# Performance work log

Hardware: AMD Instinct MI355X
Metric: run time of the kernel (lower is better)

The kernel has to match this reference:

```python
import jax, jax.numpy as jnp
import numpy as np

H_DIM = 2048
N_HEADS = 16

def setup_inputs() -> dict:
    key = jax.random.key(0)
    ks = jax.random.split(key, 9)
    B, T, C = 2, 2048, H_DIM
    scale = 1.0 / np.sqrt(C)  # lecun_normal approx
    src = jax.random.normal(ks[0], (B, T, C), dtype=jnp.float32)
    Wq = jax.random.normal(ks[1], (C, H_DIM), dtype=jnp.float32) * scale
    Wk = jax.random.normal(ks[2], (C, H_DIM), dtype=jnp.float32) * scale
    Wv = jax.random.normal(ks[3], (C, H_DIM), dtype=jnp.float32) * scale
    Wo = jax.random.normal(ks[4], (H_DIM, H_DIM), dtype=jnp.float32) * scale
    bq = jnp.zeros((H_DIM,), jnp.float32)
    bk = jnp.zeros((H_DIM,), jnp.float32)
    bv = jnp.zeros((H_DIM,), jnp.float32)
    bo = jnp.zeros((H_DIM,), jnp.float32)
    return {"src": src, "Wq": Wq, "bq": bq, "Wk": Wk, "bk": bk,
            "Wv": Wv, "bv": bv, "Wo": Wo, "bo": bo}

def reference(src, Wq, bq, Wk, bk, Wv, bv, Wo, bo):
    B, T, C = src.shape
    N = N_HEADS
    D = C // N
    def heads(x):  # [B,T,h_dim] -> [B,N,T,D]
        return x.reshape(B, T, N, D).transpose(0, 2, 1, 3)
    q = heads(src @ Wq + bq)
    k = heads(src @ Wk + bk)
    v = heads(src @ Wv + bv)
    # scaled dot-product with causal mask
    scores = jnp.einsum('bntd,bnsd->bnts', q, k) / jnp.sqrt(jnp.float32(D))
    causal = jnp.tril(jnp.ones((T, T), dtype=bool))
    scores = jnp.where(causal[None, None], scores, -jnp.inf)
    attn = jax.nn.softmax(scores, axis=-1)
    out = jnp.einsum('bnts,bnsd->bntd', attn, v)  # dropout is identity (drop_p=0)
    out = out.transpose(0, 2, 1, 3).reshape(B, T, N * D)
    return out @ Wo + bo
```

## Files before the change

kernel.cpp:

```cpp
#include <hip/hip_runtime.h>
#include <hip/hip_bf16.h>

typedef float f32x4 __attribute__((ext_vector_type(4)));
typedef __bf16 bf16x8v __attribute__((ext_vector_type(8)));
typedef __bf16 bf16x4v __attribute__((ext_vector_type(4)));
typedef unsigned uint2v __attribute__((ext_vector_type(2)));
typedef bf16x8v __attribute__((may_alias)) bf16x8;
typedef bf16x4v __attribute__((may_alias)) bf16x4;
typedef uint2v __attribute__((may_alias)) u32x2;

typedef __attribute__((address_space(1))) const void gvoid_t;
typedef __attribute__((address_space(3))) void lvoid_t;

#define DEVINL __device__ __forceinline__

#define BDIM 2
#define TDIM 2048
#define CDIM 2048
#define NHEAD 16
#define DHEAD 128
#define MROWS 4096
#define WSZ ((size_t)CDIM * CDIM)
#define XSZ ((size_t)MROWS * CDIM)

#define BARRIER_LGKM() asm volatile("s_waitcnt lgkmcnt(0)\ns_barrier" ::: "memory")

DEVINL __bf16 f2bf(float f) {
  unsigned u = __builtin_bit_cast(unsigned, f);
  u += 0x7fffu + ((u >> 16) & 1u);
  unsigned short h = (unsigned short)(u >> 16);
  return __builtin_bit_cast(__bf16, h);
}

DEVINL unsigned pk2bf_trunc(float lo, float hi) {
  return __builtin_amdgcn_perm(__builtin_bit_cast(unsigned, hi),
                               __builtin_bit_cast(unsigned, lo), 0x07060302);
}

DEVINL void gl2lds16(const void* g, void* l) {
  __builtin_amdgcn_global_load_lds((gvoid_t*)g, (lvoid_t*)l, 16, 0, 0);
}

__global__ void detect_dtype(const unsigned* __restrict__ w,
                             int* __restrict__ flag, int* __restrict__ cnt) {
  const int l = threadIdx.x;
  if (l == 0) *cnt = 0;
  const unsigned word = w[l];
  const unsigned e = (word >> 7) & 0xFFu;
  const int vote = (e >= 0x70u && e <= 0x87u) ? 1 : 0;
  const unsigned long long m = __ballot(vote);
  if (l == 0) *flag = (__popcll(m) >= 32) ? 1 : 0;
}

__global__ __launch_bounds__(256) void cvt_src(const void* __restrict__ in,
                                               __bf16* __restrict__ out,
                                               const int* __restrict__ flag,
                                               int n8) {
  const int i = blockIdx.x * 256 + threadIdx.x;
  if (i >= n8) return;
  if (*flag) {
    ((bf16x8*)out)[i] = ((const bf16x8*)in)[i];
  } else {
    const float* f = (const float*)in + (size_t)i * 8;
    bf16x8v v;
#pragma unroll
    for (int j = 0; j < 8; ++j) v[j] = f2bf(f[j]);
    ((bf16x8*)out)[i] = v;
  }
}

__global__ __launch_bounds__(256) void cvt_wt(
    const void* __restrict__ w0, const void* __restrict__ w1,
    const void* __restrict__ w2, const void* __restrict__ w3,
    __bf16* __restrict__ out, const int* __restrict__ flag) {
  __shared__ __attribute__((aligned(16))) __bf16 tile[64][68];
  const void* W = (blockIdx.z == 0) ? w0 : (blockIdx.z == 1) ? w1
                : (blockIdx.z == 2) ? w2 : w3;
  __bf16* Wt = out + (size_t)blockIdx.z * WSZ;
  const int tx = threadIdx.x & 63, ty = threadIdx.x >> 6;
  const int k0 = blockIdx.x * 64, n0 = blockIdx.y * 64;
  const int fl = *flag;
#pragma unroll
  for (int i = ty; i < 64; i += 4) {
    const size_t off = (size_t)(k0 + i) * CDIM + n0 + tx;
    const float v = fl ? (float)((const __bf16*)W)[off] : ((const float*)W)[off];
    tile[i][tx] = f2bf(v);
  }
  __syncthreads();
#pragma unroll
  for (int i = ty; i < 64; i += 4)
    Wt[(size_t)(n0 + i) * CDIM + k0 + tx] = tile[tx][i];
}

__global__ __launch_bounds__(256) void cvt_bias(
    const void* __restrict__ b0, const void* __restrict__ b1,
    const void* __restrict__ b2, const void* __restrict__ b3,
    float* __restrict__ out, const int* __restrict__ flag) {
  const int i = blockIdx.x * 256 + threadIdx.x;
  const void* b = (i < 2048) ? b0 : (i < 4096) ? b1 : (i < 6144) ? b2 : b3;
  const int idx = i & 2047;
  out[i] = (*flag) ? (float)((const __bf16*)b)[idx] : ((const float*)b)[idx];
}

__global__ __launch_bounds__(256) void gemm_qkv(
    const __bf16* __restrict__ A, const __bf16* __restrict__ Bt,
    const float* __restrict__ bias, __bf16* __restrict__ qb,
    __bf16* __restrict__ kb, __bf16* __restrict__ vtb) {
  constexpr int K = CDIM;
  __shared__ __attribute__((aligned(16))) __bf16 Als[128 * 32];
  __shared__ __attribute__((aligned(16))) __bf16 Bls[128 * 32];
  const int tid = threadIdx.x;
  const int w = tid >> 6, l = tid & 63;
  const int quad = l >> 4, l16 = l & 15;
  const int wm = (w >> 1) * 64, wn = (w & 1) * 64;
  const int m0 = blockIdx.x * 128, n0 = blockIdx.y * 128;

  f32x4 acc[4][4];
#pragma unroll
  for (int i = 0; i < 4; ++i)
#pragma unroll
    for (int j = 0; j < 4; ++j) acc[i][j] = (f32x4){0.f, 0.f, 0.f, 0.f};

  const int srow = w * 32 + (l >> 2);
  const int swz = (l & 3) ^ ((l >> 3) & 3);
  const __bf16* ga = A + (size_t)(m0 + srow) * K + swz * 8;
  const __bf16* gb = Bt + (size_t)(n0 + srow) * K + swz * 8;
  __bf16* la = Als + w * 1024;
  __bf16* lb = Bls + w * 1024;
  const int cswz = (quad ^ ((l16 >> 1) & 3)) * 8;

  for (int k0 = 0; k0 < K; k0 += 32) {
    __syncthreads();
#pragma unroll
    for (int j = 0; j < 2; ++j) {
      gl2lds16(ga + (size_t)j * 16 * K + k0, la + j * 512);
      gl2lds16(gb + (size_t)j * 16 * K + k0, lb + j * 512);
    }
    __syncthreads();
    bf16x8 af[4], bfr[4];
#pragma unroll
    for (int i = 0; i < 4; ++i)
      af[i] = *(const bf16x8*)&Als[(wm + i * 16 + l16) * 32 + cswz];
#pragma unroll
    for (int j = 0; j < 4; ++j)
      bfr[j] = *(const bf16x8*)&Bls[(wn + j * 16 + l16) * 32 + cswz];
#pragma unroll
    for (int i = 0; i < 4; ++i)
#pragma unroll
      for (int j = 0; j < 4; ++j)
        acc[i][j] = __builtin_amdgcn_mfma_f32_16x16x32_bf16(af[i], bfr[j],
                                                            acc[i][j], 0, 0, 0);
  }

  const int mat = n0 >> 11;
#pragma unroll
  for (int j = 0; j < 4; ++j) {
    const int n = n0 + wn + j * 16 + l16;
    const int nn = n & 2047;
    const int h = nn >> 7, d = nn & 127;
    const float bv = bias[n];
#pragma unroll
    for (int i = 0; i < 4; ++i) {
      const int mbase = m0 + wm + i * 16 + quad * 4;
      const int bb = mbase >> 11, t = mbase & 2047;
      if (mat == 2) {
        bf16x4v v4;
#pragma unroll
        for (int r = 0; r < 4; ++r) v4[r] = f2bf(acc[i][j][r] + bv);
        *(bf16x4*)&vtb[((size_t)(bb * NHEAD + h) * DHEAD + d) * TDIM + t] = v4;
      } else {
        __bf16* outp = (mat == 0) ? qb : kb;
#pragma unroll
        for (int r = 0; r < 4; ++r)
          outp[((size_t)(bb * NHEAD + h) * TDIM + t + r) * DHEAD + d] =
              f2bf(acc[i][j][r] + bv);
      }
    }
  }
}

__global__ __launch_bounds__(256) void gemm_out(
    const __bf16* __restrict__ A, const __bf16* __restrict__ Bt,
    const float* __restrict__ bias, void* __restrict__ outp,
    const int* __restrict__ flag) {
  constexpr int K = CDIM;
  __shared__ __attribute__((aligned(16))) __bf16 Als[128 * 32];
  __shared__ __attribute__((aligned(16))) __bf16 Bls[128 * 32];
  const int tid = threadIdx.x;
  const int w = tid >> 6, l = tid & 63;
  const int quad = l >> 4, l16 = l & 15;
  const int wm = (w >> 1) * 64, wn = (w & 1) * 64;
  const int m0 = blockIdx.x * 128, n0 = blockIdx.y * 128;
  const int ofl = *flag;

  f32x4 acc[4][4];
#pragma unroll
  for (int i = 0; i < 4; ++i)
#pragma unroll
    for (int j = 0; j < 4; ++j) acc[i][j] = (f32x4){0.f, 0.f, 0.f, 0.f};

  const int srow = w * 32 + (l >> 2);
  const int swz = (l & 3) ^ ((l >> 3) & 3);
  const __bf16* ga = A + (size_t)(m0 + srow) * K + swz * 8;
  const __bf16* gb = Bt + (size_t)(n0 + srow) * K + swz * 8;
  __bf16* la = Als + w * 1024;
  __bf16* lb = Bls + w * 1024;
  const int cswz = (quad ^ ((l16 >> 1) & 3)) * 8;

  for (int k0 = 0; k0 < K; k0 += 32) {
    __syncthreads();
#pragma unroll
    for (int j = 0; j < 2; ++j) {
      gl2lds16(ga + (size_t)j * 16 * K + k0, la + j * 512);
      gl2lds16(gb + (size_t)j * 16 * K + k0, lb + j * 512);
    }
    __syncthreads();
    bf16x8 af[4], bfr[4];
#pragma unroll
    for (int i = 0; i < 4; ++i)
      af[i] = *(const bf16x8*)&Als[(wm + i * 16 + l16) * 32 + cswz];
#pragma unroll
    for (int j = 0; j < 4; ++j)
      bfr[j] = *(const bf16x8*)&Bls[(wn + j * 16 + l16) * 32 + cswz];
#pragma unroll
    for (int i = 0; i < 4; ++i)
#pragma unroll
      for (int j = 0; j < 4; ++j)
        acc[i][j] = __builtin_amdgcn_mfma_f32_16x16x32_bf16(af[i], bfr[j],
                                                            acc[i][j], 0, 0, 0);
  }

#pragma unroll
  for (int j = 0; j < 4; ++j) {
    const int n = n0 + wn + j * 16 + l16;
    const float bv = bias[n];
#pragma unroll
    for (int i = 0; i < 4; ++i) {
#pragma unroll
      for (int r = 0; r < 4; ++r) {
        const int m = m0 + wm + i * 16 + quad * 4 + r;
        const float v = acc[i][j][r] + bv;
        if (ofl) ((__bf16*)outp)[(size_t)m * CDIM + n] = f2bf(v);
        else     ((float*)outp)[(size_t)m * CDIM + n] = v;
      }
    }
  }
}

__global__ __launch_bounds__(256, 2) void attn(
    const __bf16* __restrict__ Q, const __bf16* __restrict__ K,
    const __bf16* __restrict__ Vt, __bf16* __restrict__ ctx,
    int* __restrict__ cnt) {
  constexpr float CSC = 0.12753139726f;
  __shared__ __attribute__((aligned(16))) __bf16 Kls[64 * 128];
  __shared__ __attribute__((aligned(16))) __bf16 Vls[128 * 64];
  __shared__ __attribute__((aligned(16))) __bf16 Pls[4][32 * 64];
  __shared__ int jobLds;

  const int tid = threadIdx.x;
  const int w = tid >> 6, l = tid & 63, quad = l >> 4, l16 = l & 15;

  const int krow = tid >> 4;
  const int kcol = tid & 15;
  const int kldsoff = ((kcol ^ krow) * 8);
  const int vrow = tid >> 3;
  const int vcol = tid & 7;
  const int vldsoff = ((vcol ^ (vrow & 7)) * 8);

  for (;;) {
    __syncthreads();
    if (tid == 0) jobLds = atomicAdd(cnt, 1);
    __syncthreads();
    const int j = jobLds;
    if (j >= 512) break;
    const int qt = 15 - (j >> 5);
    const int bh = j & 31;
    const int t0w = qt * 128 + w * 32;
    const __bf16* Qbh = Q + (size_t)bh * TDIM * DHEAD;
    const __bf16* Kbh = K + (size_t)bh * TDIM * DHEAD;
    const __bf16* Vbh = Vt + (size_t)bh * TDIM * DHEAD;

    bf16x8 qf[2][4];
#pragma unroll
    for (int tt = 0; tt < 2; ++tt)
#pragma unroll
      for (int ks = 0; ks < 4; ++ks)
        qf[tt][ks] = *(const bf16x8*)(Qbh +
                     (size_t)(t0w + tt * 16 + l16) * DHEAD + ks * 32 + quad * 8);

    f32x4 oacc[8][2];
#pragma unroll
    for (int dt = 0; dt < 8; ++dt)
#pragma unroll
      for (int tt = 0; tt < 2; ++tt) oacc[dt][tt] = (f32x4){0.f, 0.f, 0.f, 0.f};
    float mrow[2] = {-1e30f, -1e30f};
    float lrow[2] = {0.f, 0.f};

    const int nsb = 2 * (qt + 1);

    bf16x8 kr[4], vr[4];
#pragma unroll
    for (int p = 0; p < 4; ++p)
      kr[p] = *(const bf16x8*)(Kbh + (size_t)(p * 16 + krow) * DHEAD + kcol * 8);
#pragma unroll
    for (int p = 0; p < 4; ++p)
      vr[p] = *(const bf16x8*)(Vbh + (size_t)(p * 32 + vrow) * TDIM + vcol * 8);

    for (int sb = 0; sb < nsb; ++sb) {
      const int s0 = sb * 64;
      BARRIER_LGKM();
#pragma unroll
      for (int p = 0; p < 4; ++p)
        *(bf16x8*)&Kls[(p * 16 + krow) * 128 + kldsoff] = kr[p];
#pragma unroll
      for (int p = 0; p < 4; ++p)
        *(bf16x8*)&Vls[(p * 32 + vrow) * 64 + vldsoff] = vr[p];
      if (sb + 1 < nsb) {
        const int s1 = s0 + 64;
#pragma unroll
        for (int p = 0; p < 4; ++p)
          kr[p] = *(const bf16x8*)(Kbh + (size_t)(s1 + p * 16 + krow) * DHEAD +
                                   kcol * 8);
#pragma unroll
        for (int p = 0; p < 4; ++p)
          vr[p] = *(const bf16x8*)(Vbh + (size_t)(p * 32 + vrow) * TDIM + s1 +
                                   vcol * 8);
      }
      BARRIER_LGKM();
      if (s0 > t0w + 31) continue;

      f32x4 sacc[4][2];
#pragma unroll
      for (int st = 0; st < 4; ++st)
#pragma unroll
        for (int tt = 0; tt < 2; ++tt) sacc[st][tt] = (f32x4){0.f, 0.f, 0.f, 0.f};
#pragma unroll
      for (int ks = 0; ks < 4; ++ks) {
        bf16x8 kf[4];
#pragma unroll
        for (int st = 0; st < 4; ++st)
          kf[st] = *(const bf16x8*)&Kls[(st * 16 + l16) * 128 +
                                        (((ks * 4 + quad) ^ l16) * 8)];
#pragma unroll
        for (int st = 0; st < 4; ++st)
#pragma unroll
          for (int tt = 0; tt < 2; ++tt)
            sacc[st][tt] = __builtin_amdgcn_mfma_f32_16x16x32_bf16(
                kf[st], qf[tt][ks], sacc[st][tt], 0, 0, 0);
      }
      if (s0 + 63 > t0w) {
#pragma unroll
        for (int st = 0; st < 4; ++st)
#pragma unroll
          for (int tt = 0; tt < 2; ++tt)
#pragma unroll
            for (int r = 0; r < 4; ++r) {
              const int s = s0 + st * 16 + quad * 4 + r;
              const int t = t0w + tt * 16 + l16;
              if (s > t) sacc[st][tt][r] = -1e30f;
            }
      }
#pragma unroll
      for (int tt = 0; tt < 2; ++tt) {
        float vm = -1e30f;
#pragma unroll
        for (int st = 0; st < 4; ++st)
#pragma unroll
          for (int r = 0; r < 4; ++r) vm = fmaxf(vm, sacc[st][tt][r]);
        vm = fmaxf(vm, __shfl_xor(vm, 16));
        vm = fmaxf(vm, __shfl_xor(vm, 32));
        const float mnew = fmaxf(mrow[tt], vm);
        if (__ballot(mnew > mrow[tt])) {
          const float alpha = exp2f((mrow[tt] - mnew) * CSC);
          lrow[tt] *= alpha;
#pragma unroll
          for (int dt = 0; dt < 8; ++dt)
#pragma unroll
            for (int r = 0; r < 4; ++r) oacc[dt][tt][r] *= alpha;
          mrow[tt] = mnew;
        }
        float rs = 0.f;
#pragma unroll
        for (int st = 0; st < 4; ++st) {
          const float p0 = exp2f((sacc[st][tt][0] - mnew) * CSC);
          const float p1 = exp2f((sacc[st][tt][1] - mnew) * CSC);
          const float p2 = exp2f((sacc[st][tt][2] - mnew) * CSC);
          const float p3 = exp2f((sacc[st][tt][3] - mnew) * CSC);
          rs += (p0 + p1) + (p2 + p3);
          u32x2 pk = {pk2bf_trunc(p0, p1), pk2bf_trunc(p2, p3)};
          *(u32x2*)&Pls[w][(tt * 16 + l16) * 64 +
                           (((st * 2 + (quad >> 1)) ^ (l16 & 7)) * 8) +
                           (quad & 1) * 4] = pk;
        }
        rs += __shfl_xor(rs, 16);
        rs += __shfl_xor(rs, 32);
        lrow[tt] += rs;
      }
      asm volatile("s_waitcnt lgkmcnt(0)" ::: "memory");
#pragma unroll
      for (int ks = 0; ks < 2; ++ks) {
        bf16x8 pf[2];
#pragma unroll
        for (int tt = 0; tt < 2; ++tt)
          pf[tt] = *(const bf16x8*)&Pls[w][(tt * 16 + l16) * 64 +
                                           (((ks * 4 + quad) ^ (l16 & 7)) * 8)];
#pragma unroll
        for (int dt = 0; dt < 8; ++dt) {
          const bf16x8 vf =
              *(const bf16x8*)&Vls[(dt * 16 + l16) * 64 +
                                   (((ks * 4 + quad) ^ (l16 & 7)) * 8)];
#pragma unroll
          for (int tt = 0; tt < 2; ++tt)
            oacc[dt][tt] = __builtin_amdgcn_mfma_f32_16x16x32_bf16(
                vf, pf[tt], oacc[dt][tt], 0, 0, 0);
        }
      }
    }

    const int b = bh >> 4, h = bh & 15;
#pragma unroll
    for (int tt = 0; tt < 2; ++tt) {
      const float rinv = 1.0f / lrow[tt];
      const int t = t0w + tt * 16 + l16;
      __bf16* cp = ctx + ((size_t)(b * TDIM + t)) * CDIM + h * DHEAD;
#pragma unroll
      for (int dt = 0; dt < 8; ++dt) {
        bf16x4v v4;
#pragma unroll
        for (int r = 0; r < 4; ++r) v4[r] = f2bf(oacc[dt][tt][r] * rinv);
        *(bf16x4*)&cp[dt * 16 + quad * 4] = v4;
      }
    }
  }
}

extern "C" void kernel_launch(void* const* d_in, const int* in_sizes, int n_in,
                              void* d_out, int out_size, void* d_ws,
                              size_t ws_size, hipStream_t stream) {
  const void* src = d_in[0];
  const void* Wq = d_in[1];
  const void* bq = d_in[2];
  const void* Wk = d_in[3];
  const void* bk = d_in[4];
  const void* Wv = d_in[5];
  const void* bv = d_in[6];
  const void* Wo = d_in[7];
  const void* bo = d_in[8];

  char* wsb = (char*)d_ws;
  int* flag = (int*)wsb;
  int* cnt = (int*)(wsb + 128);
  __bf16* srcbf = (__bf16*)(wsb + 256);
  __bf16* wqt = srcbf + XSZ;
  __bf16* wkt = wqt + WSZ;
  __bf16* wvt = wkt + WSZ;
  __bf16* wot = wvt + WSZ;
  __bf16* qb = wot + WSZ;
  __bf16* kb = qb + XSZ;
  __bf16* vtb = kb + XSZ;
  float* biasf = (float*)(vtb + XSZ);
  __bf16* ctx = srcbf;

  detect_dtype<<<1, 64, 0, stream>>>((const unsigned*)src, flag, cnt);
  cvt_src<<<4096, 256, 0, stream>>>(src, srcbf, flag, (int)(XSZ / 8));
  cvt_wt<<<dim3(32, 32, 4), 256, 0, stream>>>(Wq, Wk, Wv, Wo, wqt, flag);
  cvt_bias<<<32, 256, 0, stream>>>(bq, bk, bv, bo, biasf, flag);
  gemm_qkv<<<dim3(32, 48), 256, 0, stream>>>(srcbf, wqt, biasf, qb, kb, vtb);
  attn<<<512, 256, 0, stream>>>(qb, kb, vtb, ctx, cnt);
  gemm_out<<<dim3(32, 16), 256, 0, stream>>>(ctx, wot, biasf + 6144, d_out, flag);
}
```

Before: 428.1 us.

## Replace GEMM kernels with double-buffered 8-wave 128x256 tile GEMM

Merges the QKV and output projection GEMMs into one templated kernel that uses 512 threads, a 128x256 block tile and a K step of 64. The LDS buffers are double-buffered, and global-to-LDS loads for the next K tile are spread across four MFMA phases, with partial vmcnt waits and s_setprio around the MFMA bursts. Block indices are remapped so each XCD works on a contiguous group of N tiles, aiming for better L2 reuse. The goal is to hide memory latency and cut barrier overhead compared with the old single-buffered 32-wide K loop. The cost is higher LDS and register pressure and a more intricate synchronisation scheme.

```diff
diff --git a/kernel.cpp b/kernel.cpp
--- a/kernel.cpp
+++ b/kernel.cpp
@@ -24,6 +24,20 @@
 #define XSZ ((size_t)MROWS * CDIM)
 
 #define BARRIER_LGKM() asm volatile("s_waitcnt lgkmcnt(0)\ns_barrier" ::: "memory")
+
+#define GEMM_BAR_LGKM()                              \
+  do {                                               \
+    asm volatile("s_waitcnt lgkmcnt(0)" ::: "memory"); \
+    __builtin_amdgcn_sched_barrier(0);               \
+    __builtin_amdgcn_s_barrier();                    \
+  } while (0)
+
+#define GEMM_BAR_VM(N)                                \
+  do {                                                \
+    asm volatile("s_waitcnt vmcnt(" #N ")" ::: "memory"); \
+    __builtin_amdgcn_sched_barrier(0);                \
+    __builtin_amdgcn_s_barrier();                     \
+  } while (0)
 
 DEVINL __bf16 f2bf(float f) {
   unsigned u = __builtin_bit_cast(unsigned, f);
@@ -102,18 +116,38 @@
   out[i] = (*flag) ? (float)((const __bf16*)b)[idx] : ((const float*)b)[idx];
 }
 
-__global__ __launch_bounds__(256) void gemm_qkv(
+template <int NTN, int MODE>
+__global__ __launch_bounds__(512, 2) void gemm8p(
     const __bf16* __restrict__ A, const __bf16* __restrict__ Bt,
     const float* __restrict__ bias, __bf16* __restrict__ qb,
-    __bf16* __restrict__ kb, __bf16* __restrict__ vtb) {
+    __bf16* __restrict__ kb, __bf16* __restrict__ vtb,
+    const int* __restrict__ flag, void* __restrict__ outp) {
   constexpr int K = CDIM;
-  __shared__ __attribute__((aligned(16))) __bf16 Als[128 * 32];
-  __shared__ __attribute__((aligned(16))) __bf16 Bls[128 * 32];
+  constexpr int NKT = K / 64;
+  __shared__ __attribute__((aligned(16))) __bf16 Als[2][128 * 64];
+  __shared__ __attribute__((aligned(16))) __bf16 Bls[2][256 * 64];
+
   const int tid = threadIdx.x;
   const int w = tid >> 6, l = tid & 63;
   const int quad = l >> 4, l16 = l & 15;
-  const int wm = (w >> 1) * 64, wn = (w & 1) * 64;
-  const int m0 = blockIdx.x * 128, n0 = blockIdx.y * 128;
+  const int wm = (w >> 2) * 64, wn = (w & 3) * 64;
+
+  const int bid = blockIdx.x;
+  const int xcd = bid & 7, loc = bid >> 3;
+  const int bm = loc & 31, bn = xcd * (NTN / 8) + (loc >> 5);
+  const int m0 = bm * 128, n0 = bn * 256;
+
+  const int srow = tid >> 3;
+  const int scb = (tid & 7) ^ (srow & 7);
+  const __bf16* gA = A + (size_t)(m0 + srow) * K + scb * 8;
+  const __bf16* gB = Bt + (size_t)(n0 + srow) * K + scb * 8;
+  const int wl = w * 512;
+
+  const int aoff = (wm + l16) * 64;
+  const int boff = (wn + l16) * 64;
+  int cp[2];
+  cp[0] = ((0 + quad) ^ (l16 & 7)) * 8;
+  cp[1] = ((4 + quad) ^ (l16 & 7)) * 8;
 
   f32x4 acc[4][4];
 #pragma unroll
@@ -121,127 +155,120 @@
 #pragma unroll
     for (int j = 0; j < 4; ++j) acc[i][j] = (f32x4){0.f, 0.f, 0.f, 0.f};
 
-  const int srow = w * 32 + (l >> 2);
-  const int swz = (l & 3) ^ ((l >> 3) & 3);
-  const __bf16* ga = A + (size_t)(m0 + srow) * K + swz * 8;
-  const __bf16* gb = Bt + (size_t)(n0 + srow) * K + swz * 8;
-  __bf16* la = Als + w * 1024;
-  __bf16* lb = Bls + w * 1024;
-  const int cswz = (quad ^ ((l16 >> 1) & 3)) * 8;
-
-  for (int k0 = 0; k0 < K; k0 += 32) {
-    __syncthreads();
-#pragma unroll
-    for (int j = 0; j < 2; ++j) {
-      gl2lds16(ga + (size_t)j * 16 * K + k0, la + j * 512);
-      gl2lds16(gb + (size_t)j * 16 * K + k0, lb + j * 512);
-    }
-    __syncthreads();
-    bf16x8 af[4], bfr[4];
-#pragma unroll
-    for (int i = 0; i < 4; ++i)
-      af[i] = *(const bf16x8*)&Als[(wm + i * 16 + l16) * 32 + cswz];
-#pragma unroll
-    for (int j = 0; j < 4; ++j)
-      bfr[j] = *(const bf16x8*)&Bls[(wn + j * 16 + l16) * 32 + cswz];
-#pragma unroll
-    for (int i = 0; i < 4; ++i)
-#pragma unroll
-      for (int j = 0; j < 4; ++j)
-        acc[i][j] = __builtin_amdgcn_mfma_f32_16x16x32_bf16(af[i], bfr[j],
-                                                            acc[i][j], 0, 0, 0);
+  gl2lds16(gA, &Als[0][wl]);
+  gl2lds16(gA + (size_t)64 * K, &Als[0][4096 + wl]);
+  gl2lds16(gB, &Bls[0][wl]);
+  gl2lds16(gB + (size_t)64 * K, &Bls[0][4096 + wl]);
+  gl2lds16(gB + (size_t)128 * K, &Bls[0][8192 + wl]);
+  gl2lds16(gB + (size_t)192 * K, &Bls[0][12288 + wl]);
+  gl2lds16(gA + 64, &Als[1][wl]);
+  gl2lds16(gA + (size_t)64 * K + 64, &Als[1][4096 + wl]);
+
+#define READ_HALF(I0)                                                        \
+  _Pragma("unroll") for (int ii = 0; ii < 2; ++ii)                           \
+  _Pragma("unroll") for (int ks = 0; ks < 2; ++ks) {                         \
+    af[(I0) + ii][ks] =                                                      \
+        *(const bf16x8*)&Ab[aoff + ((I0) + ii) * 1024 + cp[ks]];             \
+    bfv[(I0) + ii][ks] =                                                     \
+        *(const bf16x8*)&Bb[boff + ((I0) + ii) * 1024 + cp[ks]];             \
   }
 
-  const int mat = n0 >> 11;
-#pragma unroll
-  for (int j = 0; j < 4; ++j) {
-    const int n = n0 + wn + j * 16 + l16;
-    const int nn = n & 2047;
-    const int h = nn >> 7, d = nn & 127;
-    const float bv = bias[n];
-#pragma unroll
-    for (int i = 0; i < 4; ++i) {
-      const int mbase = m0 + wm + i * 16 + quad * 4;
-      const int bb = mbase >> 11, t = mbase & 2047;
-      if (mat == 2) {
-        bf16x4v v4;
-#pragma unroll
-        for (int r = 0; r < 4; ++r) v4[r] = f2bf(acc[i][j][r] + bv);
-        *(bf16x4*)&vtb[((size_t)(bb * NHEAD + h) * DHEAD + d) * TDIM + t] = v4;
-      } else {
-        __bf16* outp = (mat == 0) ? qb : kb;
-#pragma unroll
-        for (int r = 0; r < 4; ++r)
-          outp[((size_t)(bb * NHEAD + h) * TDIM + t + r) * DHEAD + d] =
-              f2bf(acc[i][j][r] + bv);
-      }
-    }
+#define MFMA_QUAD(I0, J0)                                                    \
+  __builtin_amdgcn_s_setprio(1);                                            \
+  _Pragma("unroll") for (int ii = 0; ii < 2; ++ii)                           \
+  _Pragma("unroll") for (int jj = 0; jj < 2; ++jj)                           \
+  _Pragma("unroll") for (int ks = 0; ks < 2; ++ks)                           \
+      acc[(I0) + ii][(J0) + jj] = __builtin_amdgcn_mfma_f32_16x16x32_bf16(   \
+          af[(I0) + ii][ks], bfv[(J0) + jj][ks], acc[(I0) + ii][(J0) + jj],  \
+          0, 0, 0);                                                          \
+  __builtin_amdgcn_s_setprio(0);
+
+  for (int kt = 0; kt < NKT; ++kt) {
+    const __bf16* Ab = Als[kt & 1];
+    const __bf16* Bb = Bls[kt & 1];
+    if (kt + 1 < NKT) {
+      GEMM_BAR_VM(2);
+    } else {
+      GEMM_BAR_VM(0);
+    }
+
+    bf16x8 af[4][2], bfv[4][2];
+
+    READ_HALF(0)
+    if (kt + 1 < NKT) {
+      const int nb = (kt + 1) & 1;
+      gl2lds16(gB + (size_t)(kt + 1) * 64, &Bls[nb][wl]);
+      gl2lds16(gB + (size_t)64 * K + (size_t)(kt + 1) * 64,
+               &Bls[nb][4096 + wl]);
+    }
+    MFMA_QUAD(0, 0)
+    GEMM_BAR_LGKM();
+
+    READ_HALF(2)
+    if (kt + 1 < NKT) {
+      const int nb = (kt + 1) & 1;
+      gl2lds16(gB + (size_t)128 * K + (size_t)(kt + 1) * 64,
+               &Bls[nb][8192 + wl]);
+      gl2lds16(gB + (size_t)192 * K + (size_t)(kt + 1) * 64,
+               &Bls[nb][12288 + wl]);
+    }
+    MFMA_QUAD(2, 2)
+    GEMM_BAR_LGKM();
+
+    if (kt + 2 < NKT)
+      gl2lds16(gA + (size_t)(kt + 2) * 64, &Als[kt & 1][wl]);
+    MFMA_QUAD(0, 2)
+    GEMM_BAR_LGKM();
+
+    if (kt + 2 < NKT)
+      gl2lds16(gA + (size_t)64 * K + (size_t)(kt + 2) * 64,
+               &Als[kt & 1][4096 + wl]);
+    MFMA_QUAD(2, 0)
   }
-}
-
-__global__ __launch_bounds__(256) void gemm_out(
-    const __bf16* __restrict__ A, const __bf16* __restrict__ Bt,
-    const float* __restrict__ bias, void* __restrict__ outp,
-    const int* __restrict__ flag) {
-  constexpr int K = CDIM;
-  __shared__ __attribute__((aligned(16))) __bf16 Als[128 * 32];
-  __shared__ __attribute__((aligned(16))) __bf16 Bls[128 * 32];
-  const int tid = threadIdx.x;
-  const int w = tid >> 6, l = tid & 63;
-  const int quad = l >> 4, l16 = l & 15;
-  const int wm = (w >> 1) * 64, wn = (w & 1) * 64;
-  const int m0 = blockIdx.x * 128, n0 = blockIdx.y * 128;
-  const int ofl = *flag;
-
-  f32x4 acc[4][4];
-#pragma unroll
-  for (int i = 0; i < 4; ++i)
-#pragma unroll
-    for (int j = 0; j < 4; ++j) acc[i][j] = (f32x4){0.f, 0.f, 0.f, 0.f};
-
-  const int srow = w * 32 + (l >> 2);
-  const int swz = (l & 3) ^ ((l >> 3) & 3);
-  const __bf16* ga = A + (size_t)(m0 + srow) * K + swz * 8;
-  const __bf16* gb = Bt + (size_t)(n0 + srow) * K + swz * 8;
-  __bf16* la = Als + w * 1024;
-  __bf16* lb = Bls + w * 1024;
-  const int cswz = (quad ^ ((l16 >> 1) & 3)) * 8;
-
-  for (int k0 = 0; k0 < K; k0 += 32) {
-    __syncthreads();
-#pragma unroll
-    for (int j = 0; j < 2; ++j) {
-      gl2lds16(ga + (size_t)j * 16 * K + k0, la + j * 512);
-      gl2lds16(gb + (size_t)j * 16 * K + k0, lb + j * 512);
-    }
-    __syncthreads();
-    bf16x8 af[4], bfr[4];
-#pragma unroll
-    for (int i = 0; i < 4; ++i)
-      af[i] = *(const bf16x8*)&Als[(wm + i * 16 + l16) * 32 + cswz];
-#pragma unroll
-    for (int j = 0; j < 4; ++j)
-      bfr[j] = *(const bf16x8*)&Bls[(wn + j * 16 + l16) * 32 + cswz];
-#pragma unroll
-    for (int i = 0; i < 4; ++i)
-#pragma unroll
-      for (int j = 0; j < 4; ++j)
-        acc[i][j] = __builtin_amdgcn_mfma_f32_16x16x32_bf16(af[i], bfr[j],
-                                                            acc[i][j], 0, 0, 0);
-  }
-
-#pragma unroll
-  for (int j = 0; j < 4; ++j) {
-    const int n = n0 + wn + j * 16 + l16;
-    const float bv = bias[n];
-#pragma unroll
-    for (int i = 0; i < 4; ++i) {
-#pragma unroll
-      for (int r = 0; r < 4; ++r) {
-        const int m = m0 + wm + i * 16 + quad * 4 + r;
-        const float v = acc[i][j][r] + bv;
-        if (ofl) ((__bf16*)outp)[(size_t)m * CDIM + n] = f2bf(v);
-        else     ((float*)outp)[(size_t)m * CDIM + n] = v;
+#undef READ_HALF
+#undef MFMA_QUAD
+
+  if (MODE == 0) {
+    const int mat = n0 >> 11;
+#pragma unroll
+    for (int j = 0; j < 4; ++j) {
+      const int n = n0 + wn + j * 16 + l16;
+      const int nn = n & 2047;
+      const int h = nn >> 7, d = nn & 127;
+      const float bv = bias[n];
+#pragma unroll
+      for (int i = 0; i < 4; ++i) {
+        const int mbase = m0 + wm + i * 16 + quad * 4;
+        const int bb = mbase >> 11, t = mbase & 2047;
+        if (mat == 2) {
+          bf16x4v v4;
+#pragma unroll
+          for (int r = 0; r < 4; ++r) v4[r] = f2bf(acc[i][j][r] + bv);
+          *(bf16x4*)&vtb[((size_t)(bb * NHEAD + h) * DHEAD + d) * TDIM + t] = v4;
+        } else {
+          __bf16* op = (mat == 0) ? qb : kb;
+#pragma unroll
+          for (int r = 0; r < 4; ++r)
+            op[((size_t)(bb * NHEAD + h) * TDIM + t + r) * DHEAD + d] =
+                f2bf(acc[i][j][r] + bv);
+        }
+      }
+    }
+  } else {
+    const int ofl = *flag;
+#pragma unroll
+    for (int j = 0; j < 4; ++j) {
+      const int n = n0 + wn + j * 16 + l16;
+      const float bv = bias[n];
+#pragma unroll
+      for (int i = 0; i < 4; ++i) {
+#pragma unroll
+        for (int r = 0; r < 4; ++r) {
+          const int m = m0 + wm + i * 16 + quad * 4 + r;
+          const float v = acc[i][j][r] + bv;
+          if (ofl) ((__bf16*)outp)[(size_t)m * CDIM + n] = f2bf(v);
+          else     ((float*)outp)[(size_t)m * CDIM + n] = v;
+        }
       }
     }
   }
@@ -465,7 +492,9 @@
   cvt_src<<<4096, 256, 0, stream>>>(src, srcbf, flag, (int)(XSZ / 8));
   cvt_wt<<<dim3(32, 32, 4), 256, 0, stream>>>(Wq, Wk, Wv, Wo, wqt, flag);
   cvt_bias<<<32, 256, 0, stream>>>(bq, bk, bv, bo, biasf, flag);
-  gemm_qkv<<<dim3(32, 48), 256, 0, stream>>>(srcbf, wqt, biasf, qb, kb, vtb);
+  gemm8p<24, 0><<<768, 512, 0, stream>>>(srcbf, wqt, biasf, qb, kb, vtb,
+                                         nullptr, nullptr);
   attn<<<512, 256, 0, stream>>>(qb, kb, vtb, ctx, cnt);
-  gemm_out<<<dim3(32, 16), 256, 0, stream>>>(ctx, wot, biasf + 6144, d_out, flag);
-}
+  gemm8p<8, 1><<<256, 512, 0, stream>>>(ctx, wot, biasf + 6144, nullptr,
+                                        nullptr, nullptr, flag, d_out);
+}
```

Result: slower. 437.7 us (+2.2%).
